# Performance work log

Measured on AMD Instinct MI355X. Metric: run time of the kernel, lower is better.

## Reference

```python
import jax, jax.numpy as jnp
import numpy as np

B, S, H = 8, 2048, 1024
CHUNK = 64
INTER = 2048
BASE_LR = 0.01
MAX_GRAD_NORM = 1.0
EPS = 1e-6


def rmsnorm(x, w):
    return x * jax.lax.rsqrt(jnp.mean(x * x, axis=-1, keepdims=True) + EPS) * w


def mem_fwd(params, x):
    # 2-layer MLP memory with residual: x + RMSNorm(W1 @ silu(W0 @ x))
    w0, w1, ln = params
    h = jax.nn.silu(x @ w0.T)
    y = h @ w1.T
    return x + rmsnorm(y, ln)


def forward(x, wq_w, wk_w, wv_w, q_norm_w, k_norm_w, alpha_w, theta_w, eta_w, mem_w0, mem_w1, mem_ln_w):
    Bx, Sx, Hx = x.shape
    NC = Sx // CHUNK  # seq_len divisible by chunk_size here (no padding needed)
    xc = x.reshape(Bx, NC, CHUNK, Hx)
    xf = xc.reshape(Bx, NC, CHUNK * Hx)

    # adaptive coefficients per chunk
    alpha = jax.nn.sigmoid(jnp.mean(xf @ alpha_w.T, axis=0))   # (NC, 1)
    theta = jax.nn.sigmoid(xf @ theta_w.T) * BASE_LR           # (B, NC, 1) per-sample loss weights
    eta = jax.nn.sigmoid(jnp.mean(xf @ eta_w.T, axis=0))       # (NC, 1)
    beta = 1.0 - alpha

    k = rmsnorm(jax.nn.silu(xc @ wk_w.T), k_norm_w)  # (B, NC, C, H)
    v = jax.nn.silu(xc @ wv_w.T)                     # (B, NC, C, H)

    mem0 = (mem_w0, mem_w1, mem_ln_w)
    surp0 = jax.tree_util.tree_map(jnp.zeros_like, mem0)

    def step(carry, inp):
        mem, surp = carry
        k_c, v_c, th_c, eta_c, beta_c = inp  # k_c,v_c: (B,C,H); th_c: (B,1); eta_c,beta_c: (1,)

        def loss_fn(p):
            pred = mem_fwd(p, k_c)
            return jnp.mean((v_c - pred) ** 2 * th_c[:, :, None])

        grads = jax.grad(loss_fn)(mem)
        total = jnp.sqrt(sum(jnp.sum(g * g) for g in grads))
        clip = jax.lax.stop_gradient(jnp.minimum(MAX_GRAD_NORM / (total + 1e-6), 1.0))
        new_surp = tuple(eta_c * s_ - g * clip for s_, g in zip(surp, grads))
        new_mem = tuple(beta_c * m + ns for m, ns in zip(mem, new_surp))
        return (new_mem, new_surp), None

    xs = (jnp.swapaxes(k, 0, 1), jnp.swapaxes(v, 0, 1), jnp.swapaxes(theta, 0, 1), eta, beta)
    (mem_f, _), _ = jax.lax.scan(step, (mem0, surp0), xs)

    # retrieve with final memory weights
    q = rmsnorm(jax.nn.silu(x @ wq_w.T), q_norm_w)
    return mem_fwd(mem_f, q)


def setup_inputs() -> dict:
    key = jax.random.key(0)
    ks = jax.random.split(key, 9)
    s = 0.02
    return {
        "x": jax.random.normal(ks[0], (B, S, H), jnp.float32),
        "wq_w": jax.random.normal(ks[1], (H, H), jnp.float32) * s,
        "wk_w": jax.random.normal(ks[2], (H, H), jnp.float32) * s,
        "wv_w": jax.random.normal(ks[3], (H, H), jnp.float32) * s,
        "q_norm_w": jnp.ones((H,), jnp.float32),
        "k_norm_w": jnp.ones((H,), jnp.float32),
        "alpha_w": jax.random.normal(ks[4], (1, CHUNK * H), jnp.float32) * s,
        "theta_w": jax.random.normal(ks[5], (1, CHUNK * H), jnp.float32) * s,
        "eta_w": jax.random.normal(ks[6], (1, CHUNK * H), jnp.float32) * s,
        "mem_w0": jax.random.normal(ks[7], (INTER, H), jnp.float32) * s,
        "mem_w1": jax.random.normal(ks[8], (H, INTER), jnp.float32) * s,
        "mem_ln_w": jnp.ones((H,), jnp.float32),
    }


def reference(x, wq_w, wk_w, wv_w, q_norm_w, k_norm_w, alpha_w, theta_w, eta_w, mem_w0, mem_w1, mem_ln_w):
    return forward(x, wq_w, wk_w, wv_w, q_norm_w, k_norm_w, alpha_w, theta_w, eta_w, mem_w0, mem_w1, mem_ln_w)
```

## Files before the change

kernel.cpp:

```cpp
#include <hip/hip_runtime.h>

#define HD 1024
#define ID 2048
#define NCHUNK 32
#define CHUNKSZ 64
#define NB 8
#define SEQ 2048
#define ROWS 512
#define MTOT 524288.0f
#define EPSF 1e-6f

typedef unsigned short u16;
typedef unsigned int u32;
typedef short bf16x8 __attribute__((ext_vector_type(8)));
typedef float f32x4 __attribute__((ext_vector_type(4)));

#define GATHER(r, c) ((((r) >> 6) * SEQ) + ((c) * CHUNKSZ) + ((r) & 63))

__device__ __forceinline__ float sigmoidf_(float x) { return 1.f / (1.f + expf(-x)); }
__device__ __forceinline__ float siluf_(float x)    { return x / (1.f + expf(-x)); }
__device__ __forceinline__ float silu_d_(float z)   { float sg = sigmoidf_(z); return sg * (1.f + z * (1.f - sg)); }

__device__ __forceinline__ u16 f2b(float f) {
  union { float f; u32 u; } v; v.f = f;
  return (u16)((v.u + 0x7fffu + ((v.u >> 16) & 1u)) >> 16);
}
__device__ __forceinline__ float b2f(u16 b) {
  union { u32 u; float f; } v; v.u = ((u32)b) << 16; return v.f;
}
__device__ __forceinline__ u32 pack2(float a, float b) { return (u32)f2b(a) | ((u32)f2b(b) << 16); }

__device__ __forceinline__ float block_reduce_sum(float v, float* s4) {
  #pragma unroll
  for (int off = 32; off > 0; off >>= 1) v += __shfl_down(v, off);
  int lane = threadIdx.x & 63, wid = threadIdx.x >> 6;
  if (lane == 0) s4[wid] = v;
  __syncthreads();
  float r = s4[0] + s4[1] + s4[2] + s4[3];
  __syncthreads();
  return r;
}

template<bool T>
__device__ __forceinline__ void stage64(u16* S, int srow, int c16, const uint4& r0, const uint4& r1) {
  if (!T) {
// ... 1 lines not shown
    *(uint4*)(S + srow * 72 + c16 + 8) = r1;
  } else {
    const u16* e0 = (const u16*)&r0;
    const u16* e1 = (const u16*)&r1;
    #pragma unroll
    for (int e = 0; e < 8; ++e) S[(c16 + e) * 72 + srow] = e0[e];
    #pragma unroll
    for (int e = 0; e < 8; ++e) S[(c16 + 8 + e) * 72 + srow] = e1[e];
  }
}

template<bool AT, bool BT>
__device__ __forceinline__ void gemm64_db(
    f32x4 (&acc)[2][2], const u16* __restrict__ A, const u16* __restrict__ B,
    int K, int m0, int n0, int lda, int ldb, int chA, int chB,
    u16* As, u16* Bs)
{
  const int tid = threadIdx.x;
  const int lane = tid & 63, wave = tid >> 6;
  const int wr = wave >> 1, wc = wave & 1;
  const int l15 = lane & 15, q = lane >> 4;
  const int srow = tid >> 2, c16 = (tid & 3) * 16;

  const u16* Ap; size_t Astep;
  if (!AT) {
    int r = m0 + srow;
    if (chA >= 0) r = GATHER(r, chA);
    Ap = A + (size_t)r * lda + c16;
    Astep = 64;
  } else {
    Ap = A + (size_t)srow * lda + m0 + c16;
    Astep = (size_t)64 * lda;
  }
// ... 93 lines not shown
      for (int j = 0; j < 2; ++j) bg[j] = *(const bf16x8*)&Bc[(wc * 32 + j * 16 + l15) * 72 + ks * 32 + q * 8];
      #pragma unroll
      for (int i = 0; i < 2; ++i)
        #pragma unroll
        for (int j = 0; j < 2; ++j)
          acc[i][j] = __builtin_amdgcn_mfma_f32_16x16x32_bf16(af[i], bg[j], acc[i][j], 0, 0, 0);
    }
    if (t + 1 < nt) {
      stage64<false>(Ah + (cur ^ 1) * (64 * 72), srow, c16, ra0, ra1);
      stage64<BT>(Bh + (cur ^ 1) * (64 * 72), srow, c16, rb0, rb1);
    }
    cur ^= 1;
  }
}

__global__ __launch_bounds__(512) void gemm64_fwd(
    float* __restrict__ C, u16* __restrict__ Cb,
    const u16* __restrict__ A, const u16* __restrict__ B, int N, int K, int chunk)
{
  __shared__ __align__(16) u16 As[2 * 2 * 64 * 72];
  __shared__ __align__(16) u16 Bs[2 * 2 * 64 * 72];
  const int m0 = blockIdx.y * 64, n0 = blockIdx.x * 64;
  f32x4 acc[2][2] = {};
  gemm64x8<false>(acc, A, B, K, m0, n0, K, K, chunk, As, Bs);
  const int tid = threadIdx.x;
  const int half = tid >> 8, t2 = tid & 255;
  const int lane = tid & 63, w2 = t2 >> 6;
  const int wr = w2 >> 1, wc = w2 & 1;
  const int l15 = lane & 15, q = lane >> 4;
  float* Cm = (float*)As;
  __syncthreads();
  if (half) {
    #pragma unroll
    for (int i = 0; i < 2; ++i)
      #pragma unroll
      for (int j = 0; j < 2; ++j)
        #pragma unroll
        for (int t = 0; t < 4; ++t)
          Cm[(wr * 32 + i * 16 + q * 4 + t) * 66 + wc * 32 + j * 16 + l15] = acc[i][j][t];
  }
  __syncthreads();
  if (!half) {
    #pragma unroll
    for (int i = 0; i < 2; ++i) {
      int r = m0 + wr * 32 + i * 16 + q * 4;
      #pragma unroll
      for (int j = 0; j < 2; ++j) {
        int col = n0 + wc * 32 + j * 16 + l15;
        #pragma unroll
        for (int t = 0; t < 4; ++t) {
          float v = acc[i][j][t] + Cm[(wr * 32 + i * 16 + q * 4 + t) * 66 + wc * 32 + j * 16 + l15];
          size_t o = (size_t)(r + t) * N + col;
          C[o] = v;
          Cb[o] = f2b(siluf_(v));
        }
      }
    }
  }
}

__global__ __launch_bounds__(512) void gemm64_dh(
    u16* __restrict__ Cb, const u16* __restrict__ A, const u16* __restrict__ B,
    const float* __restrict__ Z, int N, int K)
{
  __shared__ __align__(16) u16 As[2 * 2 * 64 * 72];
  __shared__ __align__(16) u16 Bs[2 * 2 * 64 * 72];
  const int m0 = blockIdx.y * 64, n0 = blockIdx.x * 64;
  f32x4 acc[2][2] = {};
  gemm64x8<true>(acc, A, B, K, m0, n0, K, N, -1, As, Bs);
  const int tid = threadIdx.x;
  const int half = tid >> 8, t2 = tid & 255;
  const int lane = tid & 63, w2 = t2 >> 6;
  const int wr = w2 >> 1, wc = w2 & 1;
  const int l15 = lane & 15, q = lane >> 4;
  float* Cm = (float*)As;
  __syncthreads();
  if (half) {
    #pragma unroll
    for (int i = 0; i < 2; ++i)
      #pragma unroll
      for (int j = 0; j < 2; ++j)
        #pragma unroll
        for (int t = 0; t < 4; ++t)
          Cm[(wr * 32 + i * 16 + q * 4 + t) * 66 + wc * 32 + j * 16 + l15] = acc[i][j][t];
  }
  __syncthreads();
  if (!half) {
    #pragma unroll
    for (int i = 0; i < 2; ++i) {
      int r = m0 + wr * 32 + i * 16 + q * 4;
      #pragma unroll
      for (int j = 0; j < 2; ++j) {
        int col = n0 + wc * 32 + j * 16 + l15;
        #pragma unroll
        for (int t = 0; t < 4; ++t) {
          float v = acc[i][j][t] + Cm[(wr * 32 + i * 16 + q * 4 + t) * 66 + wc * 32 + j * 16 + l15];
          size_t o = (size_t)(r + t) * N + col;
          Cb[o] = f2b(v * silu_d_(Z[o]));
        }
      }
    }
  }
}

__global__ __launch_bounds__(256) void gemm_grads(
    float* __restrict__ Gw1, const u16* __restrict__ dY, const u16* __restrict__ hfw,
    float* __restrict__ Gw0, const u16* __restrict__ dH, const u16* __restrict__ kall,
    int c, const float* __restrict__ g, const float* __restrict__ y,
    const float* __restrict__ srow, float* __restrict__ Gln, float* __restrict__ nsqc)
{
  __shared__ __align__(16) u16 As[2 * 64 * 72];
  __shared__ __align__(16) u16 Bs[2 * 64 * 72];
  __shared__ float s4[4];
  int bid = blockIdx.x;
// ... 15 lines not shown
      float tot = 0.f;
      #pragma unroll
      for (int k = 0; k < 8; ++k) tot += part[k * 32 + tid];
      Gln[j] = tot;
      float sq = tot * tot;
      #pragma unroll
      for (int off = 16; off > 0; off >>= 1) sq += __shfl_down(sq, off);
      if (tid == 0) atomicAdd(nsqc, sq);
    }
    return;
  }
  float* C; const u16* A; const u16* B; int N, m0, n0, lda, ldb, chB;
  if (bid < 512) { A = dY; B = hfw;  C = Gw1; N = ID; lda = HD; ldb = ID; chB = -1; m0 = (bid >> 5) * 64; n0 = (bid & 31) * 64; }
  else { bid -= 512; A = dH; B = kall; C = Gw0; N = HD; lda = ID; ldb = HD; chB = c; m0 = (bid >> 4) * 64; n0 = (bid & 15) * 64; }
  f32x4 acc[2][2] = {};
  gemm64_db<true, true>(acc, A, B, ROWS, m0, n0, lda, ldb, -1, chB, As, Bs);
  const int lane = tid & 63, wave = tid >> 6;
  const int wr = wave >> 1, wc = wave & 1;
  const int l15 = lane & 15, q = lane >> 4;
  float ssq = 0.f;
  #pragma unroll
  for (int i = 0; i < 2; ++i) {
    int r = m0 + wr * 32 + i * 16 + q * 4;
    #pragma unroll
    for (int j = 0; j < 2; ++j) {
      int col = n0 + wc * 32 + j * 16 + l15;
      #pragma unroll
      for (int t = 0; t < 4; ++t) {
        float v = acc[i][j][t];
        C[(size_t)(r + t) * N + col] = v;
        ssq += v * v;
      }
    }
  }
  float tot = block_reduce_sum(ssq, s4);
  if (tid == 0) atomicAdd(nsqc, tot);
}

__global__ __launch_bounds__(512) void gemm_y32(
    float* __restrict__ C, const u16* __restrict__ A, const u16* __restrict__ B,
    int N, int K)
{
  __shared__ __align__(16) u16 As[4 * 2 * 32 * 72];
  __shared__ __align__(16) u16 Bs[4 * 2 * 64 * 72];
  const int tid = threadIdx.x;
  const int qt = tid >> 7;
  const int t2 = tid & 127;
  const int lane = tid & 63;
  const int wc = t2 >> 6;
  const int l15 = lane & 15, q = lane >> 4;
  const int m0 = blockIdx.y * 32, n0 = blockIdx.x * 64;
  const int kbase = qt * (K >> 2);

  const int arow = t2 >> 2, ac16 = (t2 & 3) * 16;
  const int brow = t2 >> 1, bc32 = (t2 & 1) * 32;
  const u16* Ap = A + (size_t)(m0 + arow) * K + kbase + ac16;
  const u16* Bp = B + (size_t)(n0 + brow) * K + kbase + bc32;
  u16* Aq = As + qt * (2 * 32 * 72);
  u16* Bq = Bs + qt * (2 * 64 * 72);

  uint4 ra0 = *(const uint4*)Ap, ra1 = *(const uint4*)(Ap + 8);
  uint4 rb0 = *(const uint4*)Bp, rb1 = *(const uint4*)(Bp + 8);
  uint4 rb2 = *(const uint4*)(Bp + 16), rb3 = *(const uint4*)(Bp + 24);
  {
    u16* Aw = Aq + arow * 72 + ac16;
    u16* Bw = Bq + brow * 72 + bc32;
    *(uint4*)Aw = ra0; *(uint4*)(Aw + 8) = ra1;
    *(uint4*)Bw = rb0; *(uint4*)(Bw + 8) = rb1;
    *(uint4*)(Bw + 16) = rb2; *(uint4*)(Bw + 24) = rb3;
  }

  f32x4 acc[2][2] = {};
  const int nt = K >> 8;
  int cur = 0;
  for (int t = 0; t < nt; ++t) {
    if (t + 1 < nt) {
      Ap += 64; Bp += 64;
      ra0 = *(const uint4*)Ap; ra1 = *(const uint4*)(Ap + 8);
      rb0 = *(const uint4*)Bp; rb1 = *(const uint4*)(Bp + 8);
      rb2 = *(const uint4*)(Bp + 16); rb3 = *(const uint4*)(Bp + 24);
    }
    __syncthreads();
    const u16* Ac = Aq + cur * (32 * 72);
    const u16* Bc = Bq + cur * (64 * 72);
    #pragma unroll
    for (int ks = 0; ks < 2; ++ks) {
      bf16x8 af[2], bg[2];
      #pragma unroll
      for (int i = 0; i < 2; ++i) af[i] = *(const bf16x8*)&Ac[(i * 16 + l15) * 72 + ks * 32 + q * 8];
      #pragma unroll
      for (int j = 0; j < 2; ++j) bg[j] = *(const bf16x8*)&Bc[(wc * 32 + j * 16 + l15) * 72 + ks * 32 + q * 8];
      #pragma unroll
      for (int i = 0; i < 2; ++i)
        #pragma unroll
        for (int j = 0; j < 2; ++j)
          acc[i][j] = __builtin_amdgcn_mfma_f32_16x16x32_bf16(af[i], bg[j], acc[i][j], 0, 0, 0);
    }
    if (t + 1 < nt) {
      u16* Aw = Aq + (cur ^ 1) * (32 * 72) + arow * 72 + ac16;
      u16* Bw = Bq + (cur ^ 1) * (64 * 72) + brow * 72 + bc32;
      *(uint4*)Aw = ra0; *(uint4*)(Aw + 8) = ra1;
      *(uint4*)Bw = rb0; *(uint4*)(Bw + 8) = rb1;
      *(uint4*)(Bw + 16) = rb2; *(uint4*)(Bw + 24) = rb3;
    }
    cur ^= 1;
  }
  float* Cm = (float*)As;
  __syncthreads();
  if (qt) {
    #pragma unroll
    for (int i = 0; i < 2; ++i)
      #pragma unroll
      for (int j = 0; j < 2; ++j)
        #pragma unroll
        for (int t = 0; t < 4; ++t)
          Cm[((qt - 1) * 32 + i * 16 + q * 4 + t) * 66 + wc * 32 + j * 16 + l15] = acc[i][j][t];
  }
  __syncthreads();
  if (!qt) {
    #pragma unroll
    for (int i = 0; i < 2; ++i) {
      int r = m0 + i * 16 + q * 4;
      #pragma unroll
      for (int j = 0; j < 2; ++j) {
        int col = n0 + wc * 32 + j * 16 + l15;
        #pragma unroll
        for (int t = 0; t < 4; ++t) {
          float v = acc[i][j][t];
          #pragma unroll
          for (int p = 0; p < 3; ++p)
            v += Cm[(p * 32 + i * 16 + q * 4 + t) * 66 + wc * 32 + j * 16 + l15];
          C[(size_t)(r + t) * N + col] = v;
        }
      }
    }
  }
}

__device__ __forceinline__ void gemm128_core(
    f32x4 (&acc)[4][4], const u16* __restrict__ A, int lda,
    const u16* __restrict__ B, int ldb, int K, int m0, int n0,
    u16* As, u16* Bs)
{
  const int tid = threadIdx.x;
  const int lane = tid & 63, wave = tid >> 6;
  const int wr = wave >> 1, wc = wave & 1;
  const int l15 = lane & 15, q = lane >> 4;
  for (int k0 = 0; k0 < K; k0 += 32) {
    #pragma unroll
    for (int it = 0; it < 2; ++it) {
      int cid = tid + it * 256;
      int row = cid >> 2, c8 = (cid & 3) * 8;
      *(uint4*)&As[row * 40 + c8] = *(const uint4*)&A[(size_t)(m0 + row) * lda + k0 + c8];
      *(uint4*)&Bs[row * 40 + c8] = *(const uint4*)&B[(size_t)(n0 + row) * ldb + k0 + c8];
    }
    __syncthreads();
    bf16x8 af[4], bg[4];
    #pragma unroll
    for (int i = 0; i < 4; ++i) af[i] = *(const bf16x8*)&As[(wr * 64 + i * 16 + l15) * 40 + q * 8];
    #pragma unroll
    for (int j = 0; j < 4; ++j) bg[j] = *(const bf16x8*)&Bs[(wc * 64 + j * 16 + l15) * 40 + q * 8];
    #pragma unroll
    for (int i = 0; i < 4; ++i)
      #pragma unroll
      for (int j = 0; j < 4; ++j)
        acc[i][j] = __builtin_amdgcn_mfma_f32_16x16x32_bf16(af[i], bg[j], acc[i][j], 0, 0, 0);
    __syncthreads();
  }
}

__global__ __launch_bounds__(256) void gemm_qkv(
    float* __restrict__ zqC, u16* __restrict__ kC, u16* __restrict__ vC,
    const u16* __restrict__ xb, const u16* __restrict__ wk,
    const u16* __restrict__ wv, const u16* __restrict__ wq)
{
  __shared__ __align__(16) u16 As[128 * 40];
  __shared__ __align__(16) u16 Bs[128 * 40];
  int f = blockIdx.x;
  int xcd = f & 7, jj = f >> 3;
  int panel = xcd + 8 * (jj / 24);
  int w = jj % 24;
  int z = w >> 3, xt = w & 7;
  int m0 = panel * 128, n0 = xt * 128;
  const u16* B = (z == 0) ? wk : ((z == 1) ? wv : wq);
  f32x4 acc[4][4] = {};
  gemm128_core(acc, xb, HD, B, HD, HD, m0, n0, As, Bs);
  const int tid = threadIdx.x;
  const int lane = tid & 63, wave = tid >> 6;
  const int wr = wave >> 1, wc = wave & 1;
  const int l15 = lane & 15, q = lane >> 4;
  #pragma unroll
  for (int i = 0; i < 4; ++i) {
    int r = m0 + wr * 64 + i * 16 + q * 4;
    #pragma unroll
    for (int j = 0; j < 4; ++j) {
      int col = n0 + wc * 64 + j * 16 + l15;
      #pragma unroll
      for (int t = 0; t < 4; ++t) {
        float v = acc[i][j][t];
        size_t o = (size_t)(r + t) * HD + col;
        if (z == 0) kC[o] = f2b(v);
        else if (z == 1) vC[o] = f2b(siluf_(v));
        else zqC[o] = v;
      }
    }
  }
}

__global__ __launch_bounds__(256) void gemm_h(
    u16* __restrict__ hC, const u16* __restrict__ A, const u16* __restrict__ B)
{
  __shared__ __align__(16) u16 As[128 * 40];
  __shared__ __align__(16) u16 Bs[128 * 40];
  int f = blockIdx.x;
  int xcd = f & 7, jj = f >> 3;
  int panel = xcd + 8 * (jj >> 4);
  int xt = jj & 15;
  int m0 = panel * 128, n0 = xt * 128;
  f32x4 acc[4][4] = {};
  gemm128_core(acc, A, HD, B, HD, HD, m0, n0, As, Bs);
  const int tid = threadIdx.x;
  const int lane = tid & 63, wave = tid >> 6;
  const int wr = wave >> 1, wc = wave & 1;
  const int l15 = lane & 15, q = lane >> 4;
  #pragma unroll
  for (int i = 0; i < 4; ++i) {
    int r = m0 + wr * 64 + i * 16 + q * 4;
    #pragma unroll
    for (int j = 0; j < 4; ++j) {
      int col = n0 + wc * 64 + j * 16 + l15;
      #pragma unroll
      for (int t = 0; t < 4; ++t)
        hC[(size_t)(r + t) * ID + col] = f2b(siluf_(acc[i][j][t]));
    }
  }
}

__global__ __launch_bounds__(256) void gemm_y2(
    float* __restrict__ C, const u16* __restrict__ A, const u16* __restrict__ B)
{
  __shared__ __align__(16) u16 As[128 * 40];
  __shared__ __align__(16) u16 Bs[128 * 40];
  int f = blockIdx.x;
  int xcd = f & 7, jj = f >> 3;
  int panel = xcd + 8 * (jj >> 3);
  int xt = jj & 7;
  int m0 = panel * 128, n0 = xt * 128;
  f32x4 acc[4][4] = {};
  gemm128_core(acc, A, ID, B, ID, ID, m0, n0, As, Bs);
  const int tid = threadIdx.x;
  const int lane = tid & 63, wave = tid >> 6;
  const int wr = wave >> 1, wc = wave & 1;
  const int l15 = lane & 15, q = lane >> 4;
  #pragma unroll
  for (int i = 0; i < 4; ++i) {
    int r = m0 + wr * 64 + i * 16 + q * 4;
    #pragma unroll
    for (int j = 0; j < 4; ++j) {
      int col = n0 + wc * 64 + j * 16 + l15;
      #pragma unroll
      for (int t = 0; t < 4; ++t)
        C[(size_t)(r + t) * HD + col] = acc[i][j][t];
    }
  }
// ... 72 lines not shown
  size_t off = (size_t)blockIdx.x * HD;
  float sv[4]; float ss = 0.f;
  #pragma unroll
  for (int i = 0; i < 4; ++i) {
    int j = i * 256 + threadIdx.x;
    float s = siluf_(buf[off + j]);
    sv[i] = s; ss += s * s;
  }
  __shared__ float s4[4];
  ss = block_reduce_sum(ss, s4);
  float rs = rsqrtf(ss / (float)HD + EPSF);
  #pragma unroll
  for (int i = 0; i < 4; ++i) {
    int j = i * 256 + threadIdx.x;
    buf[off + j] = sv[i] * rs * nw[j];
  }
}

__global__ __launch_bounds__(256) void loss_grad(
    const float* __restrict__ y, const u16* __restrict__ kall, const u16* __restrict__ vall,
    const float* __restrict__ ln, const float* __restrict__ thetaA, int c,
    float* __restrict__ g, u16* __restrict__ dYbf, float* __restrict__ srow)
{
  int r = blockIdx.x;
  size_t off = (size_t)r * HD;
  size_t goff = (size_t)GATHER(r, c) * HD;
  float th = thetaA[(r >> 6) * 32 + c];
  float yv[4], lnv[4];
  float ss = 0.f;
  #pragma unroll
  for (int i = 0; i < 4; ++i) {
    int j = i * 256 + threadIdx.x;
    yv[i] = y[off + j];
    lnv[i] = ln[j];
    ss += yv[i] * yv[i];
  }
  __shared__ float s4[4];
  ss = block_reduce_sum(ss, s4);
  float s = rsqrtf(ss / (float)HD + EPSF);
  float coef = 2.f * th / MTOT;
  float gv[4]; float t = 0.f;
  #pragma unroll
  for (int i = 0; i < 4; ++i) {
    int j = i * 256 + threadIdx.x;
    float pred = b2f(kall[goff + j]) + yv[i] * s * lnv[i];
    float gg = coef * (pred - b2f(vall[goff + j]));
    gv[i] = gg;
    g[off + j] = gg;
    t += gg * lnv[i] * yv[i];
  }
  t = block_reduce_sum(t, s4);
  float c3 = s * s * s * t * (1.f / (float)HD);
  #pragma unroll
  for (int i = 0; i < 4; ++i) {
    int j = i * 256 + threadIdx.x;
    dYbf[off + j] = f2b(s * gv[i] * lnv[i] - c3 * yv[i]);
  }
  if (threadIdx.x == 0) srow[r] = s;
}

__global__ __launch_bounds__(256) void update_all(
    float* __restrict__ mw0, float* __restrict__ sw0, const float* __restrict__ g0, u16* __restrict__ w0b,
    float* __restrict__ mw1, float* __restrict__ sw1, const float* __restrict__ g1, u16* __restrict__ w1b,
    float* __restrict__ mln, float* __restrict__ sln, const float* __restrict__ gl,
    const float* __restrict__ etaA, const float* __restrict__ betaA, int c,
    const float* __restrict__ nsqc)
{
  float clip = fminf(1.0f / (sqrtf(*nsqc) + 1e-6f), 1.0f);
  float eta = etaA[c], beta = betaA[c];
  int bid = blockIdx.x;
  if (bid < 2048) {
    float* mw; float* sw; const float* g; u16* wb; size_t i0;
    if (bid < 1024) { mw = mw1; sw = sw1; g = g1; wb = w1b; i0 = (size_t)bid * 2048; }
    else            { mw = mw0; sw = sw0; g = g0; wb = w0b; i0 = (size_t)(bid - 1024) * 2048; }
    i0 += (size_t)threadIdx.x * 8;
    u16 bb[8];
    #pragma unroll
    for (int h = 0; h < 2; ++h) {
      size_t i = i0 + h * 4;
      float4 s = *(float4*)&sw[i];
      float4 gg = *(const float4*)&g[i];
      float4 m = *(float4*)&mw[i];
      s.x = eta * s.x - clip * gg.x; m.x = beta * m.x + s.x;
      s.y = eta * s.y - clip * gg.y; m.y = beta * m.y + s.y;
      s.z = eta * s.z - clip * gg.z; m.z = beta * m.z + s.z;
      s.w = eta * s.w - clip * gg.w; m.w = beta * m.w + s.w;
      *(float4*)&sw[i] = s;
      *(float4*)&mw[i] = m;
      bb[h * 4 + 0] = f2b(m.x); bb[h * 4 + 1] = f2b(m.y);
      bb[h * 4 + 2] = f2b(m.z); bb[h * 4 + 3] = f2b(m.w);
    }
    *(uint4*)&wb[i0] = *(uint4*)bb;
  } else {
    int i = threadIdx.x * 4;
    #pragma unroll
    for (int k = 0; k < 4; ++k) {
      float ns = eta * sln[i + k] - clip * gl[i + k];
      sln[i + k] = ns;
      mln[i + k] = beta * mln[i + k] + ns;
    }
  }
}

__global__ __launch_bounds__(256) void final_out_kernel(
    float* outp, const float* __restrict__ y2, const float* __restrict__ ln)
{
  size_t off = (size_t)blockIdx.x * HD;
  float qv[4], yv[4];
  float ss2 = 0.f;
  #pragma unroll
  for (int i = 0; i < 4; ++i) {
    int j = i * 256 + threadIdx.x;
    qv[i] = outp[off + j];
    yv[i] = y2[off + j];
    ss2 += yv[i] * yv[i];
// ... 75 lines not shown
  coeff_kernel<<<1, 256, 0, stream>>>(dotA, dotT, dotE, betaA, etaA, thetaA);
  gemm_qkv<<<3072, 256, 0, stream>>>(out, k_all, v_all, x_bf, wk_bf, wv_bf, wq_bf);
  post_norm_kb<<<NB * SEQ, 256, 0, stream>>>(k_all, kn);
  post_norm_qf<<<NB * SEQ, 256, 0, stream>>>(out, qn);
  hipMemcpyAsync(memW0, w0i, (size_t)ID * HD * 4, hipMemcpyDeviceToDevice, stream);
  hipMemcpyAsync(memW1, w1i, (size_t)HD * ID * 4, hipMemcpyDeviceToDevice, stream);
  hipMemcpyAsync(memLn, lni, (size_t)HD * 4, hipMemcpyDeviceToDevice, stream);
  hipMemsetAsync(surpW0, 0, (size_t)ID * HD * 2 * 4, stream);
  hipMemsetAsync(surpLn, 0, HD * 4, stream);
  hipMemsetAsync(nsq, 0, 64 * 4, stream);

  for (int c = 0; c < NCHUNK; ++c) {
    gemm64_fwd<<<dim3(ID / 64, ROWS / 64), 512, 0, stream>>>(
        zfw, hfw_bf, k_all, W0_bf, ID, HD, c);
    gemm_y32<<<dim3(HD / 64, ROWS / 32), 512, 0, stream>>>(ybuf, hfw_bf, W1_bf, HD, ID);
    loss_grad<<<ROWS, 256, 0, stream>>>(ybuf, k_all, v_all, memLn, thetaA, c, gbuf, dY_bf, srow);
    gemm64_dh<<<dim3(ID / 64, ROWS / 64), 512, 0, stream>>>(
        dH_bf, dY_bf, W1_bf, zfw, ID, HD);
    gemm_grads<<<1056, 256, 0, stream>>>(
        Gw1, dY_bf, hfw_bf, Gw0, dH_bf, k_all, c, gbuf, ybuf, srow, Gln, nsq + c);
    update_all<<<2049, 256, 0, stream>>>(
        memW0, surpW0, Gw0, W0_bf, memW1, surpW1, Gw1, W1_bf,
        memLn, surpLn, Gln, etaA, betaA, c, nsq + c);
  }

  u16*   qb_bf = k_all;
  u16*   h_bf  = v_all;
  float* y2    = surpW0;
  conv_f2b<<<(NB * SEQ * HD) / 1024, 256, 0, stream>>>(qb_bf, out, NB * SEQ * HD);
  for (int blk = 0; blk < 2; ++blk) {
    gemm_h<<<1024, 256, 0, stream>>>(h_bf, qb_bf + (size_t)blk * 8192 * HD, W0_bf);
    gemm_y2<<<512, 256, 0, stream>>>(y2, h_bf, W1_bf);
    final_out_kernel<<<8192, 256, 0, stream>>>(out + (size_t)blk * 8192 * HD, y2, memLn);
// ... 3 lines not shown
```

Measured before the change: 3.106 ms.

## Fuse loss gradient into dH GEMM and double-buffer 128-tile GEMMs

Merges the per-row loss/RMSNorm-backward kernel with the dH = dY·W1 GEMM. Each block recomputes dY for its 64 rows into shared memory and multiplies it by a 64-column slice of W1, so one launch and a global round trip of dY are removed from each chunk step. The cost is redundant recomputation of dY across the 32 column blocks and large shared memory use (about 134KB per block). Separately, the 128x128 GEMM core used for QKV and final retrieval now uses register-prefetched double-buffered LDS to overlap loads with MFMA.

New measurement: 7.176 ms. +131.1%, slower.

```diff
diff --git a/kernel.cpp b/kernel.cpp
--- a/kernel.cpp
+++ b/kernel.cpp
@@ -29,6 +29,10 @@
   union { u32 u; float f; } v; v.u = ((u32)b) << 16; return v.f;
 }
 __device__ __forceinline__ u32 pack2(float a, float b) { return (u32)f2b(a) | ((u32)f2b(b) << 16); }
+__device__ __forceinline__ float4 b2f4(uint2 p) {
+  return make_float4(b2f((u16)(p.x & 0xffff)), b2f((u16)(p.x >> 16)),
+                     b2f((u16)(p.y & 0xffff)), b2f((u16)(p.y >> 16)));
+}
 
 __device__ __forceinline__ float block_reduce_sum(float v, float* s4) {
   #pragma unroll
@@ -60,9 +64,8 @@
 __device__ __forceinline__ void gemm64_db(
     f32x4 (&acc)[2][2], const u16* __restrict__ A, const u16* __restrict__ B,
     int K, int m0, int n0, int lda, int ldb, int chA, int chB,
-    u16* As, u16* Bs)
-{
-  const int tid = threadIdx.x;
+    int tid, u16* As, u16* Bs)
+{
   const int lane = tid & 63, wave = tid >> 6;
   const int wr = wave >> 1, wc = wave & 1;
   const int l15 = lane & 15, q = lane >> 4;
@@ -186,21 +189,13 @@
   }
 }
 
-__global__ __launch_bounds__(512) void gemm64_fwd(
-    float* __restrict__ C, u16* __restrict__ Cb,
-    const u16* __restrict__ A, const u16* __restrict__ B, int N, int K, int chunk)
-{
-  __shared__ __align__(16) u16 As[2 * 2 * 64 * 72];
-  __shared__ __align__(16) u16 Bs[2 * 2 * 64 * 72];
-  const int m0 = blockIdx.y * 64, n0 = blockIdx.x * 64;
-  f32x4 acc[2][2] = {};
-  gemm64x8<false>(acc, A, B, K, m0, n0, K, K, chunk, As, Bs);
-  const int tid = threadIdx.x;
+__device__ __forceinline__ void merge_fwd(
+    f32x4 (&acc)[2][2], float* C, u16* Cb, int N, int m0, int n0, float* Cm, int tid)
+{
   const int half = tid >> 8, t2 = tid & 255;
   const int lane = tid & 63, w2 = t2 >> 6;
   const int wr = w2 >> 1, wc = w2 & 1;
   const int l15 = lane & 15, q = lane >> 4;
-  float* Cm = (float*)As;
   __syncthreads();
   if (half) {
     #pragma unroll
@@ -231,45 +226,241 @@
   }
 }
 
-__global__ __launch_bounds__(512) void gemm64_dh(
-    u16* __restrict__ Cb, const u16* __restrict__ A, const u16* __restrict__ B,
-    const float* __restrict__ Z, int N, int K)
+__global__ __launch_bounds__(512) void gemm64_fwd(
+    float* __restrict__ C, u16* __restrict__ Cb,
+    const u16* __restrict__ A, const u16* __restrict__ B, int N, int K, int chunk)
 {
   __shared__ __align__(16) u16 As[2 * 2 * 64 * 72];
   __shared__ __align__(16) u16 Bs[2 * 2 * 64 * 72];
   const int m0 = blockIdx.y * 64, n0 = blockIdx.x * 64;
   f32x4 acc[2][2] = {};
-  gemm64x8<true>(acc, A, B, K, m0, n0, K, N, -1, As, Bs);
+  gemm64x8<false>(acc, A, B, K, m0, n0, K, K, chunk, As, Bs);
+  merge_fwd(acc, C, Cb, N, m0, n0, (float*)As, threadIdx.x);
+}
+
+__device__ __forceinline__ void y32_body(
+    float* __restrict__ C, const u16* __restrict__ A, const u16* __restrict__ B,
+    int N, int K, int m0, int n0, u16* As, u16* Bs)
+{
   const int tid = threadIdx.x;
-  const int half = tid >> 8, t2 = tid & 255;
-  const int lane = tid & 63, w2 = t2 >> 6;
-  const int wr = w2 >> 1, wc = w2 & 1;
+  const int qt = tid >> 7;
+  const int t2 = tid & 127;
+  const int lane = tid & 63;
+  const int wc = t2 >> 6;
   const int l15 = lane & 15, q = lane >> 4;
+  const int kbase = qt * (K >> 2);
+
+  const int arow = t2 >> 2, ac16 = (t2 & 3) * 16;
+  const int brow = t2 >> 1, bc32 = (t2 & 1) * 32;
+  const u16* Ap = A + (size_t)(m0 + arow) * K + kbase + ac16;
+  const u16* Bp = B + (size_t)(n0 + brow) * K + kbase + bc32;
+  u16* Aq = As + qt * (2 * 32 * 72);
+  u16* Bq = Bs + qt * (2 * 64 * 72);
+
+  uint4 ra0 = *(const uint4*)Ap, ra1 = *(const uint4*)(Ap + 8);
+  uint4 rb0 = *(const uint4*)Bp, rb1 = *(const uint4*)(Bp + 8);
+  uint4 rb2 = *(const uint4*)(Bp + 16), rb3 = *(const uint4*)(Bp + 24);
+  {
+    u16* Aw = Aq + arow * 72 + ac16;
+    u16* Bw = Bq + brow * 72 + bc32;
+    *(uint4*)Aw = ra0; *(uint4*)(Aw + 8) = ra1;
+    *(uint4*)Bw = rb0; *(uint4*)(Bw + 8) = rb1;
+    *(uint4*)(Bw + 16) = rb2; *(uint4*)(Bw + 24) = rb3;
+  }
+
+  f32x4 acc[2][2] = {};
+  const int nt = K >> 8;
+  int cur = 0;
+  for (int t = 0; t < nt; ++t) {
+    if (t + 1 < nt) {
+      Ap += 64; Bp += 64;
+      ra0 = *(const uint4*)Ap; ra1 = *(const uint4*)(Ap + 8);
+      rb0 = *(const uint4*)Bp; rb1 = *(const uint4*)(Bp + 8);
+      rb2 = *(const uint4*)(Bp + 16); rb3 = *(const uint4*)(Bp + 24);
+    }
+    __syncthreads();
+    const u16* Ac = Aq + cur * (32 * 72);
+    const u16* Bc = Bq + cur * (64 * 72);
+    #pragma unroll
+    for (int ks = 0; ks < 2; ++ks) {
+      bf16x8 af[2], bg[2];
+      #pragma unroll
+      for (int i = 0; i < 2; ++i) af[i] = *(const bf16x8*)&Ac[(i * 16 + l15) * 72 + ks * 32 + q * 8];
+      #pragma unroll
+      for (int j = 0; j < 2; ++j) bg[j] = *(const bf16x8*)&Bc[(wc * 32 + j * 16 + l15) * 72 + ks * 32 + q * 8];
+      #pragma unroll
+      for (int i = 0; i < 2; ++i)
+        #pragma unroll
+        for (int j = 0; j < 2; ++j)
+          acc[i][j] = __builtin_amdgcn_mfma_f32_16x16x32_bf16(af[i], bg[j], acc[i][j], 0, 0, 0);
+    }
+    if (t + 1 < nt) {
+      u16* Aw = Aq + (cur ^ 1) * (32 * 72) + arow * 72 + ac16;
+      u16* Bw = Bq + (cur ^ 1) * (64 * 72) + brow * 72 + bc32;
+      *(uint4*)Aw = ra0; *(uint4*)(Aw + 8) = ra1;
+      *(uint4*)Bw = rb0; *(uint4*)(Bw + 8) = rb1;
+      *(uint4*)(Bw + 16) = rb2; *(uint4*)(Bw + 24) = rb3;
+    }
+    cur ^= 1;
+  }
   float* Cm = (float*)As;
   __syncthreads();
-  if (half) {
+  if (qt) {
     #pragma unroll
     for (int i = 0; i < 2; ++i)
       #pragma unroll
       for (int j = 0; j < 2; ++j)
         #pragma unroll
         for (int t = 0; t < 4; ++t)
-          Cm[(wr * 32 + i * 16 + q * 4 + t) * 66 + wc * 32 + j * 16 + l15] = acc[i][j][t];
+          Cm[((qt - 1) * 32 + i * 16 + q * 4 + t) * 66 + wc * 32 + j * 16 + l15] = acc[i][j][t];
   }
   __syncthreads();
-  if (!half) {
+  if (!qt) {
     #pragma unroll
     for (int i = 0; i < 2; ++i) {
-      int r = m0 + wr * 32 + i * 16 + q * 4;
+      int r = m0 + i * 16 + q * 4;
       #pragma unroll
       for (int j = 0; j < 2; ++j) {
         int col = n0 + wc * 32 + j * 16 + l15;
         #pragma unroll
         for (int t = 0; t < 4; ++t) {
-          float v = acc[i][j][t] + Cm[(wr * 32 + i * 16 + q * 4 + t) * 66 + wc * 32 + j * 16 + l15];
-          size_t o = (size_t)(r + t) * N + col;
-          Cb[o] = f2b(v * silu_d_(Z[o]));
+          float v = acc[i][j][t];
+          #pragma unroll
+          for (int p = 0; p < 3; ++p)
+            v += Cm[(p * 32 + i * 16 + q * 4 + t) * 66 + wc * 32 + j * 16 + l15];
+          C[(size_t)(r + t) * N + col] = v;
         }
+      }
+    }
+  }
+}
+
+__global__ __launch_bounds__(512) void gemm_y32(
+    float* __restrict__ C, const u16* __restrict__ A, const u16* __restrict__ B,
+    int N, int K)
+{
+  __shared__ __align__(16) u16 As[4 * 2 * 32 * 72];
+  __shared__ __align__(16) u16 Bs[4 * 2 * 64 * 72];
+  y32_body(C, A, B, N, K, blockIdx.y * 32, blockIdx.x * 64, As, Bs);
+}
+
+__global__ __launch_bounds__(512) void loss_dh(
+    const float* __restrict__ y, const u16* __restrict__ kall, const u16* __restrict__ vall,
+    const float* __restrict__ ln, const float* __restrict__ thetaA, int c,
+    float* __restrict__ g, u16* __restrict__ dYbf, float* __restrict__ srow,
+    u16* __restrict__ dH, const float* __restrict__ Z, const u16* __restrict__ W1)
+{
+  __shared__ __align__(16) u16 dYs[64 * 1048];
+  __shared__ __align__(16) u16 Bs[2 * 64 * 72];
+  const int tid = threadIdx.x;
+  const int rg = blockIdx.x >> 5, ct = blockIdx.x & 31;
+
+  {
+    const int lr = tid >> 3;
+    const int g8 = tid & 7;
+    const int r  = rg * 64 + lr;
+    const size_t off  = (size_t)r * HD;
+    const size_t goff = (size_t)(rg * SEQ + c * CHUNKSZ + lr) * HD;
+    const float th = thetaA[rg * 32 + c];
+    const int c0 = g8 * 128;
+
+    float ss = 0.f;
+    for (int i = 0; i < 32; ++i) {
+      float4 yv = *(const float4*)&y[off + c0 + i * 4];
+      ss += yv.x * yv.x + yv.y * yv.y + yv.z * yv.z + yv.w * yv.w;
+    }
+    ss += __shfl_xor(ss, 1); ss += __shfl_xor(ss, 2); ss += __shfl_xor(ss, 4);
+    float s = rsqrtf(ss / (float)HD + EPSF);
+    float coef = 2.f * th / MTOT;
+
+    float t = 0.f;
+    for (int i = 0; i < 32; ++i) {
+      int j = c0 + i * 4;
+      float4 yv = *(const float4*)&y[off + j];
+      float4 kv = b2f4(*(const uint2*)&kall[goff + j]);
+      float4 vv = b2f4(*(const uint2*)&vall[goff + j]);
+      float4 lv = *(const float4*)&ln[j];
+      float g0 = coef * ((kv.x + yv.x * s * lv.x) - vv.x);
+      float g1 = coef * ((kv.y + yv.y * s * lv.y) - vv.y);
+      float g2 = coef * ((kv.z + yv.z * s * lv.z) - vv.z);
+      float g3 = coef * ((kv.w + yv.w * s * lv.w) - vv.w);
+      t += g0 * lv.x * yv.x + g1 * lv.y * yv.y + g2 * lv.z * yv.z + g3 * lv.w * yv.w;
+      if (ct == 0) *(float4*)&g[off + j] = make_float4(g0, g1, g2, g3);
+    }
+    t += __shfl_xor(t, 1); t += __shfl_xor(t, 2); t += __shfl_xor(t, 4);
+    float c3 = s * s * s * t * (1.f / (float)HD);
+
+    for (int i = 0; i < 32; ++i) {
+      int j = c0 + i * 4;
+      float4 yv = *(const float4*)&y[off + j];
+      float4 kv = b2f4(*(const uint2*)&kall[goff + j]);
+      float4 vv = b2f4(*(const uint2*)&vall[goff + j]);
+      float4 lv = *(const float4*)&ln[j];
+      float g0 = coef * ((kv.x + yv.x * s * lv.x) - vv.x);
+      float g1 = coef * ((kv.y + yv.y * s * lv.y) - vv.y);
+      float g2 = coef * ((kv.z + yv.z * s * lv.z) - vv.z);
+      float g3 = coef * ((kv.w + yv.w * s * lv.w) - vv.w);
+      uint2 pk;
+      pk.x = pack2(s * g0 * lv.x - c3 * yv.x, s * g1 * lv.y - c3 * yv.y);
+      pk.y = pack2(s * g2 * lv.z - c3 * yv.z, s * g3 * lv.w - c3 * yv.w);
+      *(uint2*)&dYs[lr * 1048 + j] = pk;
+      if (ct == 0) *(uint2*)&dYbf[off + j] = pk;
+    }
+    if (g8 == 0 && ct == 0) srow[r] = s;
+  }
+  __syncthreads();
+
+  {
+    const int lane = tid & 63, wave = tid >> 6;
+    const int wr = wave >> 2, wc = wave & 3;
+    const int l15 = lane & 15, q = lane >> 4;
+    const int kr = tid >> 3, g8 = tid & 7;
+    const int n0 = ct * 64, m0 = rg * 64;
+
+    const u16* Bp = W1 + (size_t)kr * ID + n0 + g8 * 8;
+    uint4 rb = *(const uint4*)Bp;
+    {
+      const u16* e = (const u16*)&rb;
+      #pragma unroll
+      for (int eI = 0; eI < 8; ++eI) Bs[(g8 * 8 + eI) * 72 + kr] = e[eI];
+    }
+    f32x4 acc[2] = {};
+    int cur = 0;
+    for (int t = 0; t < 16; ++t) {
+      if (t + 1 < 16) {
+        Bp += (size_t)64 * ID;
+        rb = *(const uint4*)Bp;
+      }
+      __syncthreads();
+      const u16* Bc = Bs + cur * (64 * 72);
+      const int kb = t * 64;
+      #pragma unroll
+      for (int ks = 0; ks < 2; ++ks) {
+        bf16x8 af[2], bg;
+        #pragma unroll
+        for (int i = 0; i < 2; ++i)
+          af[i] = *(const bf16x8*)&dYs[(wr * 32 + i * 16 + l15) * 1048 + kb + ks * 32 + q * 8];
+        bg = *(const bf16x8*)&Bc[(wc * 16 + l15) * 72 + ks * 32 + q * 8];
+        #pragma unroll
+        for (int i = 0; i < 2; ++i)
+          acc[i] = __builtin_amdgcn_mfma_f32_16x16x32_bf16(af[i], bg, acc[i], 0, 0, 0);
+      }
+      if (t + 1 < 16) {
+        u16* Bw = Bs + (cur ^ 1) * (64 * 72);
+        const u16* e = (const u16*)&rb;
+        #pragma unroll
+        for (int eI = 0; eI < 8; ++eI) Bw[(g8 * 8 + eI) * 72 + kr] = e[eI];
+      }
+      cur ^= 1;
+    }
+    #pragma unroll
+    for (int i = 0; i < 2; ++i) {
+      int r = m0 + wr * 32 + i * 16 + q * 4;
+      int col = n0 + wc * 16 + l15;
+      #pragma unroll
+      for (int t4 = 0; t4 < 4; ++t4) {
+        size_t o = (size_t)(r + t4) * ID + col;
+        dH[o] = f2b(acc[i][t4] * silu_d_(Z[o]));
       }
     }
   }
@@ -315,7 +506,7 @@
   if (bid < 512) { A = dY; B = hfw;  C = Gw1; N = ID; lda = HD; ldb = ID; chB = -1; m0 = (bid >> 5) * 64; n0 = (bid & 31) * 64; }
   else { bid -= 512; A = dH; B = kall; C = Gw0; N = HD; lda = ID; ldb = HD; chB = c; m0 = (bid >> 4) * 64; n0 = (bid & 15) * 64; }
   f32x4 acc[2][2] = {};
-  gemm64_db<true, true>(acc, A, B, ROWS, m0, n0, lda, ldb, -1, chB, As, Bs);
+  gemm64_db<true, true>(acc, A, B, ROWS, m0, n0, lda, ldb, -1, chB, tid, As, Bs);
   const int lane = tid & 63, wave = tid >> 6;
   const int wr = wave >> 1, wc = wave & 1;
   const int l15 = lane & 15, q = lane >> 4;
@@ -338,107 +529,62 @@
   if (tid == 0) atomicAdd(nsqc, tot);
 }
 
-__global__ __launch_bounds__(512) void gemm_y32(
-    float* __restrict__ C, const u16* __restrict__ A, const u16* __restrict__ B,
-    int N, int K)
-{
-  __shared__ __align__(16) u16 As[4 * 2 * 32 * 72];
-  __shared__ __align__(16) u16 Bs[4 * 2 * 64 * 72];
-  const int tid = threadIdx.x;
-  const int qt = tid >> 7;
-  const int t2 = tid & 127;
-  const int lane = tid & 63;
-  const int wc = t2 >> 6;
-  const int l15 = lane & 15, q = lane >> 4;
-  const int m0 = blockIdx.y * 32, n0 = blockIdx.x * 64;
-  const int kbase = qt * (K >> 2);
-
-  const int arow = t2 >> 2, ac16 = (t2 & 3) * 16;
-  const int brow = t2 >> 1, bc32 = (t2 & 1) * 32;
-  const u16* Ap = A + (size_t)(m0 + arow) * K + kbase + ac16;
-  const u16* Bp = B + (size_t)(n0 + brow) * K + kbase + bc32;
-  u16* Aq = As + qt * (2 * 32 * 72);
-  u16* Bq = Bs + qt * (2 * 64 * 72);
-
-  uint4 ra0 = *(const uint4*)Ap, ra1 = *(const uint4*)(Ap + 8);
-  uint4 rb0 = *(const uint4*)Bp, rb1 = *(const uint4*)(Bp + 8);
-  uint4 rb2 = *(const uint4*)(Bp + 16), rb3 = *(const uint4*)(Bp + 24);
-  {
-    u16* Aw = Aq + arow * 72 + ac16;
-    u16* Bw = Bq + brow * 72 + bc32;
-    *(uint4*)Aw = ra0; *(uint4*)(Aw + 8) = ra1;
-    *(uint4*)Bw = rb0; *(uint4*)(Bw + 8) = rb1;
-    *(uint4*)(Bw + 16) = rb2; *(uint4*)(Bw + 24) = rb3;
-  }
-
-  f32x4 acc[2][2] = {};
-  const int nt = K >> 8;
-  int cur = 0;
-  for (int t = 0; t < nt; ++t) {
-    if (t + 1 < nt) {
-      Ap += 64; Bp += 64;
-      ra0 = *(const uint4*)Ap; ra1 = *(const uint4*)(Ap + 8);
-      rb0 = *(const uint4*)Bp; rb1 = *(const uint4*)(Bp + 8);
-      rb2 = *(const uint4*)(Bp + 16); rb3 = *(const uint4*)(Bp + 24);
-    }
-    __syncthreads();
-    const u16* Ac = Aq + cur * (32 * 72);
-    const u16* Bc = Bq + cur * (64 * 72);
-    #pragma unroll
-    for (int ks = 0; ks < 2; ++ks) {
-      bf16x8 af[2], bg[2];
-      #pragma unroll
-      for (int i = 0; i < 2; ++i) af[i] = *(const bf16x8*)&Ac[(i * 16 + l15) * 72 + ks * 32 + q * 8];
-      #pragma unroll
-      for (int j = 0; j < 2; ++j) bg[j] = *(const bf16x8*)&Bc[(wc * 32 + j * 16 + l15) * 72 + ks * 32 + q * 8];
-      #pragma unroll
-      for (int i = 0; i < 2; ++i)
-        #pragma unroll
-        for (int j = 0; j < 2; ++j)
-          acc[i][j] = __builtin_amdgcn_mfma_f32_16x16x32_bf16(af[i], bg[j], acc[i][j], 0, 0, 0);
-    }
-    if (t + 1 < nt) {
-      u16* Aw = Aq + (cur ^ 1) * (32 * 72) + arow * 72 + ac16;
-      u16* Bw = Bq + (cur ^ 1) * (64 * 72) + brow * 72 + bc32;
-      *(uint4*)Aw = ra0; *(uint4*)(Aw + 8) = ra1;
-      *(uint4*)Bw = rb0; *(uint4*)(Bw + 8) = rb1;
-      *(uint4*)(Bw + 16) = rb2; *(uint4*)(Bw + 24) = rb3;
-    }
-    cur ^= 1;
-  }
-  float* Cm = (float*)As;
-  __syncthreads();
-  if (qt) {
-    #pragma unroll
-    for (int i = 0; i < 2; ++i)
-      #pragma unroll
-      for (int j = 0; j < 2; ++j)
-        #pragma unroll
-        for (int t = 0; t < 4; ++t)
-          Cm[((qt - 1) * 32 + i * 16 + q * 4 + t) * 66 + wc * 32 + j * 16 + l15] = acc[i][j][t];
-  }
-  __syncthreads();
-  if (!qt) {
-    #pragma unroll
-    for (int i = 0; i < 2; ++i) {
-      int r = m0 + i * 16 + q * 4;
-      #pragma unroll
-      for (int j = 0; j < 2; ++j) {
-        int col = n0 + wc * 32 + j * 16 + l15;
-        #pragma unroll
-        for (int t = 0; t < 4; ++t) {
-          float v = acc[i][j][t];
-          #pragma unroll
-          for (int p = 0; p < 3; ++p)
-            v += Cm[(p * 32 + i * 16 + q * 4 + t) * 66 + wc * 32 + j * 16 + l15];
-          C[(size_t)(r + t) * N + col] = v;
-        }
-      }
-    }
-  }
-}
-
-__device__ __forceinline__ void gemm128_core(
+__device__ __forceinline__ void update_wslice(
+    int bid, int t,
+    float* mw0, float* sw0, const float* g0, u16* w0b,
+    float* mw1, float* sw1, const float* g1, u16* w1b,
+    float eta, float beta, float clip)
+{
+  float* mw; float* sw; const float* g; u16* wb; size_t i0;
+  if (bid < 1024) { mw = mw1; sw = sw1; g = g1; wb = w1b; i0 = (size_t)bid * 2048; }
+  else            { mw = mw0; sw = sw0; g = g0; wb = w0b; i0 = (size_t)(bid - 1024) * 2048; }
+  i0 += (size_t)t * 8;
+  u16 bb[8];
+  #pragma unroll
+  for (int h = 0; h < 2; ++h) {
+    size_t i = i0 + h * 4;
+    float4 s = *(float4*)&sw[i];
+    float4 gg = *(const float4*)&g[i];
+    float4 m = *(float4*)&mw[i];
+    s.x = eta * s.x - clip * gg.x; m.x = beta * m.x + s.x;
+    s.y = eta * s.y - clip * gg.y; m.y = beta * m.y + s.y;
+    s.z = eta * s.z - clip * gg.z; m.z = beta * m.z + s.z;
+    s.w = eta * s.w - clip * gg.w; m.w = beta * m.w + s.w;
+    *(float4*)&sw[i] = s;
+    *(float4*)&mw[i] = m;
+    bb[h * 4 + 0] = f2b(m.x); bb[h * 4 + 1] = f2b(m.y);
+    bb[h * 4 + 2] = f2b(m.z); bb[h * 4 + 3] = f2b(m.w);
+  }
+  *(uint4*)&wb[i0] = *(uint4*)bb;
+}
+
+__device__ __forceinline__ void update_ln(
+    int t, float* mln, float* sln, const float* gl, float eta, float beta, float clip)
+{
+  int i = t * 4;
+  #pragma unroll
+  for (int k = 0; k < 4; ++k) {
+    float ns = eta * sln[i + k] - clip * gl[i + k];
+    sln[i + k] = ns;
+    mln[i + k] = beta * mln[i + k] + ns;
+  }
+}
+
+__global__ __launch_bounds__(256) void update_all(
+    float* __restrict__ mw0, float* __restrict__ sw0, const float* __restrict__ g0, u16* __restrict__ w0b,
+    float* __restrict__ mw1, float* __restrict__ sw1, const float* __restrict__ g1, u16* __restrict__ w1b,
+    float* __restrict__ mln, float* __restrict__ sln, const float* __restrict__ gl,
+    const float* __restrict__ etaA, const float* __restrict__ betaA, int c,
+    const float* __restrict__ nsqc)
+{
+  float clip = fminf(1.0f / (sqrtf(*nsqc) + 1e-6f), 1.0f);
+  float eta = etaA[c], beta = betaA[c];
+  int bid = blockIdx.x;
+  if (bid < 2048) update_wslice(bid, threadIdx.x, mw0, sw0, g0, w0b, mw1, sw1, g1, w1b, eta, beta, clip);
+  else update_ln(threadIdx.x, mln, sln, gl, eta, beta, clip);
+}
+
+__device__ __forceinline__ void gemm128_db(
     f32x4 (&acc)[4][4], const u16* __restrict__ A, int lda,
     const u16* __restrict__ B, int ldb, int K, int m0, int n0,
     u16* As, u16* Bs)
@@ -447,26 +593,50 @@
   const int lane = tid & 63, wave = tid >> 6;
   const int wr = wave >> 1, wc = wave & 1;
   const int l15 = lane & 15, q = lane >> 4;
-  for (int k0 = 0; k0 < K; k0 += 32) {
-    #pragma unroll
-    for (int it = 0; it < 2; ++it) {
-      int cid = tid + it * 256;
-      int row = cid >> 2, c8 = (cid & 3) * 8;
-      *(uint4*)&As[row * 40 + c8] = *(const uint4*)&A[(size_t)(m0 + row) * lda + k0 + c8];
-      *(uint4*)&Bs[row * 40 + c8] = *(const uint4*)&B[(size_t)(n0 + row) * ldb + k0 + c8];
+  const int row0 = tid >> 2, c8 = (tid & 3) * 8;
+
+  const u16* Ap0 = A + (size_t)(m0 + row0) * lda + c8;
+  const u16* Ap1 = Ap0 + (size_t)64 * lda;
+  const u16* Bp0 = B + (size_t)(n0 + row0) * ldb + c8;
+  const u16* Bp1 = Bp0 + (size_t)64 * ldb;
+
+  uint4 a0 = *(const uint4*)Ap0, a1 = *(const uint4*)Ap1;
+  uint4 b0 = *(const uint4*)Bp0, b1 = *(const uint4*)Bp1;
+  *(uint4*)&As[row0 * 40 + c8] = a0;
+  *(uint4*)&As[(row0 + 64) * 40 + c8] = a1;
+  *(uint4*)&Bs[row0 * 40 + c8] = b0;
+  *(uint4*)&Bs[(row0 + 64) * 40 + c8] = b1;
+
+  const int nt = K >> 5;
+  int cur = 0;
+  for (int t = 0; t < nt; ++t) {
+    if (t + 1 < nt) {
+      int k1 = (t + 1) * 32;
+      a0 = *(const uint4*)(Ap0 + k1); a1 = *(const uint4*)(Ap1 + k1);
+      b0 = *(const uint4*)(Bp0 + k1); b1 = *(const uint4*)(Bp1 + k1);
     }
     __syncthreads();
+    const u16* Ac = As + cur * (128 * 40);
+    const u16* Bc = Bs + cur * (128 * 40);
     bf16x8 af[4], bg[4];
     #pragma unroll
-    for (int i = 0; i < 4; ++i) af[i] = *(const bf16x8*)&As[(wr * 64 + i * 16 + l15) * 40 + q * 8];
-    #pragma unroll
-    for (int j = 0; j < 4; ++j) bg[j] = *(const bf16x8*)&Bs[(wc * 64 + j * 16 + l15) * 40 + q * 8];
+    for (int i = 0; i < 4; ++i) af[i] = *(const bf16x8*)&Ac[(wr * 64 + i * 16 + l15) * 40 + q * 8];
+    #pragma unroll
+    for (int j = 0; j < 4; ++j) bg[j] = *(const bf16x8*)&Bc[(wc * 64 + j * 16 + l15) * 40 + q * 8];
     #pragma unroll
     for (int i = 0; i < 4; ++i)
       #pragma unroll
       for (int j = 0; j < 4; ++j)
         acc[i][j] = __builtin_amdgcn_mfma_f32_16x16x32_bf16(af[i], bg[j], acc[i][j], 0, 0, 0);
-    __syncthreads();
+    if (t + 1 < nt) {
+      u16* Aw = As + (cur ^ 1) * (128 * 40);
+      u16* Bw = Bs + (cur ^ 1) * (128 * 40);
+      *(uint4*)&Aw[row0 * 40 + c8] = a0;
+      *(uint4*)&Aw[(row0 + 64) * 40 + c8] = a1;
+      *(uint4*)&Bw[row0 * 40 + c8] = b0;
+      *(uint4*)&Bw[(row0 + 64) * 40 + c8] = b1;
+    }
+    cur ^= 1;
   }
 }
 
@@ -475,8 +645,8 @@
     const u16* __restrict__ xb, const u16* __restrict__ wk,
     const u16* __restrict__ wv, const u16* __restrict__ wq)
 {
-  __shared__ __align__(16) u16 As[128 * 40];
-  __shared__ __align__(16) u16 Bs[128 * 40];
+  __shared__ __align__(16) u16 As[2 * 128 * 40];
+  __shared__ __align__(16) u16 Bs[2 * 128 * 40];
   int f = blockIdx.x;
   int xcd = f & 7, jj = f >> 3;
   int panel = xcd + 8 * (jj / 24);
@@ -485,7 +655,7 @@
   int m0 = panel * 128, n0 = xt * 128;
   const u16* B = (z == 0) ? wk : ((z == 1) ? wv : wq);
   f32x4 acc[4][4] = {};
-  gemm128_core(acc, xb, HD, B, HD, HD, m0, n0, As, Bs);
+  gemm128_db(acc, xb, HD, B, HD, HD, m0, n0, As, Bs);
   const int tid = threadIdx.x;
   const int lane = tid & 63, wave = tid >> 6;
   const int wr = wave >> 1, wc = wave & 1;
@@ -511,15 +681,15 @@
 __global__ __launch_bounds__(256) void gemm_h(
     u16* __restrict__ hC, const u16* __restrict__ A, const u16* __restrict__ B)
 {
-  __shared__ __align__(16) u16 As[128 * 40];
-  __shared__ __align__(16) u16 Bs[128 * 40];
+  __shared__ __align__(16) u16 As[2 * 128 * 40];
+  __shared__ __align__(16) u16 Bs[2 * 128 * 40];
   int f = blockIdx.x;
   int xcd = f & 7, jj = f >> 3;
   int panel = xcd + 8 * (jj >> 4);
   int xt = jj & 15;
   int m0 = panel * 128, n0 = xt * 128;
   f32x4 acc[4][4] = {};
-  gemm128_core(acc, A, HD, B, HD, HD, m0, n0, As, Bs);
+  gemm128_db(acc, A, HD, B, HD, HD, m0, n0, As, Bs);
   const int tid = threadIdx.x;
   const int lane = tid & 63, wave = tid >> 6;
   const int wr = wave >> 1, wc = wave & 1;
@@ -540,15 +710,15 @@
 __global__ __launch_bounds__(256) void gemm_y2(
     float* __restrict__ C, const u16* __restrict__ A, const u16* __restrict__ B)
 {
-  __shared__ __align__(16) u16 As[128 * 40];
-  __shared__ __align__(16) u16 Bs[128 * 40];
+  __shared__ __align__(16) u16 As[2 * 128 * 40];
+  __shared__ __align__(16) u16 Bs[2 * 128 * 40];
   int f = blockIdx.x;
   int xcd = f & 7, jj = f >> 3;
   int panel = xcd + 8 * (jj >> 3);
   int xt = jj & 7;
   int m0 = panel * 128, n0 = xt * 128;
   f32x4 acc[4][4] = {};
-  gemm128_core(acc, A, ID, B, ID, ID, m0, n0, As, Bs);
+  gemm128_db(acc, A, ID, B, ID, ID, m0, n0, As, Bs);
   const int tid = threadIdx.x;
   const int lane = tid & 63, wave = tid >> 6;
   const int wr = wave >> 1, wc = wave & 1;
@@ -651,91 +821,6 @@
   for (int i = 0; i < 4; ++i) {
     int j = i * 256 + threadIdx.x;
     buf[off + j] = sv[i] * rs * nw[j];
-  }
-}
-
-__global__ __launch_bounds__(256) void loss_grad(
-    const float* __restrict__ y, const u16* __restrict__ kall, const u16* __restrict__ vall,
-    const float* __restrict__ ln, const float* __restrict__ thetaA, int c,
-    float* __restrict__ g, u16* __restrict__ dYbf, float* __restrict__ srow)
-{
-  int r = blockIdx.x;
-  size_t off = (size_t)r * HD;
-  size_t goff = (size_t)GATHER(r, c) * HD;
-  float th = thetaA[(r >> 6) * 32 + c];
-  float yv[4], lnv[4];
-  float ss = 0.f;
-  #pragma unroll
-  for (int i = 0; i < 4; ++i) {
-    int j = i * 256 + threadIdx.x;
-    yv[i] = y[off + j];
-    lnv[i] = ln[j];
-    ss += yv[i] * yv[i];
-  }
-  __shared__ float s4[4];
-  ss = block_reduce_sum(ss, s4);
-  float s = rsqrtf(ss / (float)HD + EPSF);
-  float coef = 2.f * th / MTOT;
-  float gv[4]; float t = 0.f;
-  #pragma unroll
-  for (int i = 0; i < 4; ++i) {
-    int j = i * 256 + threadIdx.x;
-    float pred = b2f(kall[goff + j]) + yv[i] * s * lnv[i];
-    float gg = coef * (pred - b2f(vall[goff + j]));
-    gv[i] = gg;
-    g[off + j] = gg;
-    t += gg * lnv[i] * yv[i];
-  }
-  t = block_reduce_sum(t, s4);
-  float c3 = s * s * s * t * (1.f / (float)HD);
-  #pragma unroll
-  for (int i = 0; i < 4; ++i) {
-    int j = i * 256 + threadIdx.x;
-    dYbf[off + j] = f2b(s * gv[i] * lnv[i] - c3 * yv[i]);
-  }
-  if (threadIdx.x == 0) srow[r] = s;
-}
-
-__global__ __launch_bounds__(256) void update_all(
-    float* __restrict__ mw0, float* __restrict__ sw0, const float* __restrict__ g0, u16* __restrict__ w0b,
-    float* __restrict__ mw1, float* __restrict__ sw1, const float* __restrict__ g1, u16* __restrict__ w1b,
-    float* __restrict__ mln, float* __restrict__ sln, const float* __restrict__ gl,
-    const float* __restrict__ etaA, const float* __restrict__ betaA, int c,
-    const float* __restrict__ nsqc)
-{
-  float clip = fminf(1.0f / (sqrtf(*nsqc) + 1e-6f), 1.0f);
-  float eta = etaA[c], beta = betaA[c];
-  int bid = blockIdx.x;
-  if (bid < 2048) {
-    float* mw; float* sw; const float* g; u16* wb; size_t i0;
-    if (bid < 1024) { mw = mw1; sw = sw1; g = g1; wb = w1b; i0 = (size_t)bid * 2048; }
-    else            { mw = mw0; sw = sw0; g = g0; wb = w0b; i0 = (size_t)(bid - 1024) * 2048; }
-    i0 += (size_t)threadIdx.x * 8;
-    u16 bb[8];
-    #pragma unroll
-    for (int h = 0; h < 2; ++h) {
-      size_t i = i0 + h * 4;
-      float4 s = *(float4*)&sw[i];
-      float4 gg = *(const float4*)&g[i];
-      float4 m = *(float4*)&mw[i];
-      s.x = eta * s.x - clip * gg.x; m.x = beta * m.x + s.x;
-      s.y = eta * s.y - clip * gg.y; m.y = beta * m.y + s.y;
-      s.z = eta * s.z - clip * gg.z; m.z = beta * m.z + s.z;
-      s.w = eta * s.w - clip * gg.w; m.w = beta * m.w + s.w;
-      *(float4*)&sw[i] = s;
-      *(float4*)&mw[i] = m;
-      bb[h * 4 + 0] = f2b(m.x); bb[h * 4 + 1] = f2b(m.y);
-      bb[h * 4 + 2] = f2b(m.z); bb[h * 4 + 3] = f2b(m.w);
-    }
-    *(uint4*)&wb[i0] = *(uint4*)bb;
-  } else {
-    int i = threadIdx.x * 4;
-    #pragma unroll
-    for (int k = 0; k < 4; ++k) {
-      float ns = eta * sln[i + k] - clip * gl[i + k];
-      sln[i + k] = ns;
-      mln[i + k] = beta * mln[i + k] + ns;
-    }
   }
 }
 
@@ -841,9 +926,8 @@
     gemm64_fwd<<<dim3(ID / 64, ROWS / 64), 512, 0, stream>>>(
         zfw, hfw_bf, k_all, W0_bf, ID, HD, c);
     gemm_y32<<<dim3(HD / 64, ROWS / 32), 512, 0, stream>>>(ybuf, hfw_bf, W1_bf, HD, ID);
-    loss_grad<<<ROWS, 256, 0, stream>>>(ybuf, k_all, v_all, memLn, thetaA, c, gbuf, dY_bf, srow);
-    gemm64_dh<<<dim3(ID / 64, ROWS / 64), 512, 0, stream>>>(
-        dH_bf, dY_bf, W1_bf, zfw, ID, HD);
+    loss_dh<<<256, 512, 0, stream>>>(
+        ybuf, k_all, v_all, memLn, thetaA, c, gbuf, dY_bf, srow, dH_bf, zfw, W1_bf);
     gemm_grads<<<1056, 256, 0, stream>>>(
         Gw1, dY_bf, hfw_bf, Gw0, dH_bf, k_all, c, gbuf, ybuf, srow, Gln, nsq + c);
     update_all<<<2049, 256, 0, stream>>>(
```
